# Optimization experiments

Measured on AMD Instinct MI355X. Metric: run time of the kernel, lower is better.

Reference implementation:

```python
import jax, jax.numpy as jnp
import numpy as np

B, H, W = 8, 640, 640
THRESH = 0.6       # self.threshold in Pnet_post
NMS_IOU = 0.3      # iou threshold passed in post_data_Pnet
MAX_DET = 128      # fixed detection budget (padded greedy NMS)


def _tffix(x):
    # tf fix(): floor toward zero
    return jnp.where(x >= 0, jnp.floor(x), jnp.ceil(x))


def _rec2square(rect):
    # rect: [N,5] (x1,y1,x2,y2,score) -> squared boxes
    x1, y1, x2, y2, s = rect[:, 0], rect[:, 1], rect[:, 2], rect[:, 3], rect[:, 4]
    w = x2 - x1
    h = y2 - y1
    l = jnp.maximum(w, h)
    nx1 = x1 + w * 0.5 - l * 0.5
    ny1 = y1 + h * 0.5 - l * 0.5
    return jnp.stack([nx1, ny1, nx1 + l, ny1 + l, s], axis=1)


def _greedy_nms(rect, valid):
    # rect: [N,5]; valid: [N] bool (score >= THRESH). Sequential greedy NMS
    # (highest score first, suppress iou > NMS_IOU), padded to MAX_DET rows.
    x1, y1, x2, y2 = rect[:, 0], rect[:, 1], rect[:, 2], rect[:, 3]
    area = (x2 - x1 + 1.0) * (y2 - y1 + 1.0)
    s0 = jnp.where(valid, rect[:, 4], -jnp.inf)

    def step(s, _):
        i = jnp.argmax(s)
        alive = jnp.isfinite(s[i])
        xx1 = jnp.maximum(x1[i], x1)
        yy1 = jnp.maximum(y1[i], y1)
        xx2 = jnp.minimum(x2[i], x2)
        yy2 = jnp.minimum(y2[i], y2)
        inter = jnp.maximum(0.0, xx2 - xx1 + 1.0) * jnp.maximum(0.0, yy2 - yy1 + 1.0)
        iou = inter / (area[i] + area - inter)
        s_next = jnp.where(iou > NMS_IOU, -jnp.inf, s).at[i].set(-jnp.inf)
        s_next = jnp.where(alive, s_next, s)
        return s_next, (i, alive)

    _, (picks, alive) = jax.lax.scan(step, s0, None, length=MAX_DET)
    out = rect[picks]                       # [MAX_DET,5]
    return jnp.where(alive[:, None], out, 0.0)


def _post_single(cls, roi, scale, h_raw, w_raw):
    # cls: [H,W,2], roi: [H,W,4], scale/h_raw/w_raw: scalars
    h, w = cls.shape[0], cls.shape[1]
    score = cls[:, :, 1].T                  # [W,H] == Cls_pro[...,0]
    offset = jnp.transpose(roi, (1, 0, 2))  # [W,H,4] == stacked dx1..dx4
    out_side = max(w, h)
    stride = 0.0 if out_side == 1 else (2.0 * out_side + 11.0 - 12.0) / (out_side - 1.0)
    sc = 1.0 / scale                        # scale arg of _cls_bb2rect is 1/scale
    ii = jnp.broadcast_to(jnp.arange(w, dtype=jnp.float32)[:, None], (w, h))
    jj = jnp.broadcast_to(jnp.arange(h, dtype=jnp.float32)[None, :], (w, h))
    idx = jnp.stack([ii, jj], axis=-1)      # [W,H,2] grid coords (thresh_index)
    bb1 = _tffix(stride * idx * sc)
    bb2 = _tffix((stride * idx + 11.0) * sc)
    box = jnp.concatenate([bb1, bb2], axis=-1) + offset * 12.0 * sc  # [W,H,4]
    rect = jnp.concatenate([box, score[..., None]], axis=-1).reshape(-1, 5)
    rect = _rec2square(rect)
    # pick_rect: clip to image, swap inverted corners
    x1 = jnp.maximum(0.0, rect[:, 0])
    y1 = jnp.maximum(0.0, rect[:, 1])
    x2 = jnp.minimum(w_raw, rect[:, 2])
    y2 = jnp.minimum(h_raw, rect[:, 3])
    inv = (x1 > x2) | (y1 > y2)
    fx1 = jnp.where(inv, jnp.minimum(x1, x2), x1)
    fy1 = jnp.where(inv, jnp.minimum(y1, y2), y1)
    fx2 = jnp.where(inv, jnp.maximum(x1, x2), x2)
    fy2 = jnp.where(inv, jnp.maximum(y1, y2), y2)
    pick = jnp.stack([fx1, fy1, fx2, fy2, rect[:, 4]], axis=1)
    valid = score.reshape(-1) >= THRESH     # dynamic threshold -> mask
    return _greedy_nms(pick, valid)


def setup_inputs() -> dict:
    key = jax.random.key(0)
    k1, k2, k3 = jax.random.split(key, 3)
    classifier = jax.random.uniform(k1, (B, H, W, 2), dtype=jnp.float32)
    bbox_regress = jax.random.normal(k2, (B, H, W, 4), dtype=jnp.float32) * 0.1
    scale = jax.random.uniform(k3, (B,), dtype=jnp.float32, minval=0.4, maxval=1.0)
    height_raw = jnp.full((B, 1), 1500.0, dtype=jnp.float32)
    width_raw = jnp.full((B, 1), 1500.0, dtype=jnp.float32)
    return {"classifier": classifier, "bbox_regress": bbox_regress,
            "scale": scale, "height_raw": height_raw, "width_raw": width_raw}


def reference(classifier, bbox_regress, scale, height_raw, width_raw):
    # -> [B, MAX_DET, 5]; rows beyond #detections are zero
    return jax.vmap(_post_single)(classifier, bbox_regress, scale,
                                  height_raw[:, 0], width_raw[:, 0])
```

## Files before the change

### kernel.cpp

```cpp
#include <hip/hip_runtime.h>

#define Bn 8
#define Hn 640
#define Wn 640
#define CELLS (Hn*Wn)
#define NBIN 2048
#define HB 16
#define CB 32
#define NT 5
#define TCAP 1024
#define TSTEP 832u
#define MAXD 128
#define TSTAGE 192

#define WS_CUT_BYTE 256
#define WS_PART_BYTE 512
#define WS_KEYS_BYTE (512 + Bn*HB*NBIN*2)

__global__ void k_hist(const float4* __restrict__ cls4, unsigned short* __restrict__ part) {
    __shared__ unsigned h[NBIN];
    int b = blockIdx.y, blk = blockIdx.x, tid = threadIdx.x;
    for (int p = tid; p < NBIN; p += 256) h[p] = 0u;
    __syncthreads();
    const float4* src = cls4 + ((size_t)b * CELLS + blk * (CELLS / HB)) / 2;
    for (int k = 0; k < (CELLS / HB / 2) / 256; ++k) {
        float4 v = src[k * 256 + tid];
        if (v.y >= 0.6f) {
            int bin = min((int)((v.y - 0.6f) * 5120.0f), NBIN - 1);
            atomicAdd(&h[bin], 1u);
        }
        if (v.w >= 0.6f) {
            int bin = min((int)((v.w - 0.6f) * 5120.0f), NBIN - 1);
            atomicAdd(&h[bin], 1u);
        }
    }
    __syncthreads();
    unsigned short* dst = part + (size_t)(b * HB + blk) * NBIN;
    for (int p = tid; p < NBIN; p += 256) dst[p] = (unsigned short)h[p];
}

__global__ void k_cut(const unsigned short* __restrict__ part, float* __restrict__ cutv,
                      unsigned* __restrict__ cnt) {
    __shared__ unsigned h[NBIN];
    __shared__ int best[NT];
    int b = blockIdx.x, tid = threadIdx.x;
    const int Q = NBIN / 256;
    unsigned acc[Q];
    for (int q = 0; q < Q; ++q) acc[q] = 0u;
    for (int blk = 0; blk < HB; ++blk) {
        const unsigned short* src = part + (size_t)(b * HB + blk) * NBIN;
        for (int q = 0; q < Q; ++q) acc[q] += src[q * 256 + tid];
    }
    for (int q = 0; q < Q; ++q) h[q * 256 + tid] = acc[q];
    if (tid < NT) best[tid] = 0;
    if (tid < 8) cnt[b * 8 + tid] = 0u;
    __syncthreads();
    for (int off = 1; off < NBIN; off <<= 1) {
        unsigned v[Q];
        for (int q = 0; q < Q; ++q) {
            int p = q * 256 + tid;
            v[q] = h[p] + ((p + off < NBIN) ? h[p + off] : 0u);
        }
        __syncthreads();
        for (int q = 0; q < Q; ++q) h[q * 256 + tid] = v[q];
        __syncthreads();
    }
    for (int t = 0; t < NT; ++t) {
        unsigned tgt = TSTEP * (unsigned)(t + 1);
        for (int q = 0; q < Q; ++q) {
            int p = q * 256 + tid;
            if (h[p] >= tgt && (p == NBIN - 1 || h[p + 1] < tgt)) best[t] = p;
        }
    }
    __syncthreads();
    if (tid < NT) cutv[b * 8 + tid] = 0.6f + (float)best[tid] * (0.4f / (float)NBIN);
}

__global__ void k_compact(const float4* __restrict__ cls4, const float* __restrict__ cutv_g,
                          unsigned* __restrict__ cnt, unsigned long long* __restrict__ keys) {
    __shared__ unsigned long long buf[NT][TSTAGE];
    __shared__ unsigned lcnt[NT], gbase[NT];
    int b = blockIdx.y, blk = blockIdx.x, tid = threadIdx.x;
    float c0 = cutv_g[b * 8 + 0], c1 = cutv_g[b * 8 + 1], cmid = cutv_g[b * 8 + 2],
          c3 = cutv_g[b * 8 + 3], c4 = cutv_g[b * 8 + 4];
    if (tid < NT) lcnt[tid] = 0u;
    __syncthreads();
    int cellbase = blk * (CELLS / CB);
    const float4* src = cls4 + ((size_t)b * CELLS + cellbase) / 2;
    for (int k = 0; k < (CELLS / CB / 2) / 256; ++k) {
        float4 v = src[k * 256 + tid];
        int mm = cellbase + (k * 256 + tid) * 2;
        #pragma unroll
        for (int half = 0; half < 2; ++half) {
            float s = half ? v.w : v.y;
            if (s >= c4) {
                int t = (s < c0) + (s < c1) + (s < cmid) + (s < c3);
                unsigned idx = atomicAdd(&lcnt[t], 1u);
                if (idx < TSTAGE) {
                    int m2 = mm + half;
                    int i = m2 % Wn, j = m2 / Wn;
                    unsigned n = (unsigned)(i * Hn + j);
                    buf[t][idx] = ((unsigned long long)__float_as_uint(s) << 32) |
                                  (unsigned long long)(~n);
                }
            }
        }
    }
    __syncthreads();
    if (tid < NT) gbase[tid] = atomicAdd(&cnt[b * 8 + tid], min(lcnt[tid], (unsigned)TSTAGE));
    __syncthreads();
    for (int t = 0; t < NT; ++t) {
        unsigned tot = min(lcnt[t], (unsigned)TSTAGE);
        for (unsigned i = tid; i < tot; i += 256) {
            unsigned slot = gbase[t] + i;
            if (slot < TCAP)
                keys[((size_t)b * NT + t) * TCAP + slot] = buf[t][i];
        }
    }
}

__device__ __forceinline__ void make_box(int n, float sc, float WR, float HR,
                                         const float4* __restrict__ roi4b,
                                         float& fx1, float& fy1, float& fx2, float& fy2) {
    const float stride = (float)(1279.0 / 639.0);
    int i = n / Hn, j = n % Hn;
    float fi = (float)i, fj = (float)j;
    float b1x = truncf((stride * fi) * sc);
    float b1y = truncf((stride * fj) * sc);
    float b2x = truncf((stride * fi + 11.0f) * sc);
    float b2y = truncf((stride * fj + 11.0f) * sc);
    float4 off = roi4b[j * Wn + i];
    float x1 = b1x + (off.x * 12.0f) * sc;
    float y1 = b1y + (off.y * 12.0f) * sc;
    float x2 = b2x + (off.z * 12.0f) * sc;
    float y2 = b2y + (off.w * 12.0f) * sc;
    float w = x2 - x1, h = y2 - y1;
    float l = fmaxf(w, h);
    float nx1 = x1 + w * 0.5f - l * 0.5f;
    float ny1 = y1 + h * 0.5f - l * 0.5f;
    float nx2 = nx1 + l, ny2 = ny1 + l;
    float cx1 = fmaxf(0.0f, nx1), cy1 = fmaxf(0.0f, ny1);
    float cx2 = fminf(WR, nx2),   cy2 = fminf(HR, ny2);
    bool inv = (cx1 > cx2) || (cy1 > cy2);
    fx1 = inv ? fminf(cx1, cx2) : cx1;
    fy1 = inv ? fminf(cy1, cy2) : cy1;
    fx2 = inv ? fmaxf(cx1, cx2) : cx2;
    fy2 = inv ? fmaxf(cy1, cy2) : cy2;
}

__device__ __forceinline__ void wave_phases64(unsigned long long* ks, int chunkbase,
                                              int k, int jstart) {
    int lane = threadIdx.x & 63;
    for (int j = jstart; j > 0; j >>= 1) {
        int p = chunkbase + lane;
        int ixj = p ^ j;
        if (ixj > p) {
            unsigned long long a = ks[p], c = ks[ixj];
            bool descBlk = ((p & k) == 0);
            if (descBlk ? (a < c) : (a > c)) { ks[p] = c; ks[ixj] = a; }
        }
        asm volatile("s_waitcnt lgkmcnt(0)" ::: "memory");
    }
}

__launch_bounds__(1024)
__global__ void k_nms(const float4* __restrict__ roi4, const float* __restrict__ scale,
                      const float* __restrict__ hraw, const float* __restrict__ wraw,
                      const unsigned* __restrict__ cnt,
                      const unsigned long long* __restrict__ keys_g,
                      float* __restrict__ out) {
    __shared__ unsigned long long ks[TCAP];
    __shared__ float4 bx[TCAP];
    __shared__ float4 abox[MAXD];
    __shared__ float aarea[MAXD], ascore[MAXD];
    __shared__ int sn_acc;
    int b = blockIdx.x, tid = threadIdx.x;
    int wave = tid >> 6, lane = tid & 63;
    int chunkbase = wave * 64;

    if (tid == 0) sn_acc = 0;

    float sc = 1.0f / scale[b];
    float WR = wraw[b], HR = hraw[b];
    const float4* roi4b = roi4 + (size_t)b * CELLS;

    int n_acc = 0;

    for (int t = 0; t < NT; ++t) {
        __syncthreads();
        if (sn_acc >= MAXD) break;
        int mt = (int)min(cnt[b * 8 + t], (unsigned)TCAP);
        ks[tid] = (tid < mt) ? keys_g[((size_t)b * NT + t) * TCAP + tid] : 0ULL;
        __syncthreads();

        if (mt > 1) {
            for (int k = 2; k <= 64; k <<= 1)
                wave_phases64(ks, chunkbase, k, k >> 1);
            __syncthreads();
            for (int k = 128; k <= TCAP; k <<= 1) {
                for (int j = k >> 1; j >= 64; j >>= 1) {
                    int p = tid, ixj = p ^ j;
                    if (ixj > p) {
                        unsigned long long a = ks[p], c = ks[ixj];
                        bool descBlk = ((p & k) == 0);
                        if (descBlk ? (a < c) : (a > c)) { ks[p] = c; ks[ixj] = a; }
                    }
                    __syncthreads();
                }
                wave_phases64(ks, chunkbase, k, 32);
                __syncthreads();
            }
        }

        if (tid < mt) {
            unsigned n = ~(unsigned)ks[tid];
            float fx1, fy1, fx2, fy2;
            make_box((int)n, sc, WR, HR, roi4b, fx1, fy1, fx2, fy2);
            bx[tid] = make_float4(fx1, fy1, fx2, fy2);
        }
        __syncthreads();

        if (tid < 64 && mt > 0) {
            int pos = 0;
            while (pos < mt && n_acc < MAXD) {
                int myp = pos + lane;
                bool has = myp < mt;
                unsigned long long key = has ? ks[myp] : 0ULL;
                float s = __uint_as_float((unsigned)(key >> 32));
                float4 bb0 = bx[has ? myp : 0];
                float fx1 = bb0.x, fy1 = bb0.y, fx2 = bb0.z, fy2 = bb0.w;
                float area = (fx2 - fx1 + 1.0f) * (fy2 - fy1 + 1.0f);
                bool rejected = !has;
                for (int k2 = 0; k2 < n_acc; ++k2) {
                    float4 bb = abox[k2];
                    float va = aarea[k2];
                    float iw = fminf(fx2, bb.z) - fmaxf(fx1, bb.x) + 1.0f;
                    float ih = fminf(fy2, bb.w) - fmaxf(fy1, bb.y) + 1.0f;
                    float inter = fmaxf(0.0f, iw) * fmaxf(0.0f, ih);
                    float iou = inter / (area + va - inter);
                    rejected |= (iou > 0.3f);
                }
                unsigned long long active = __ballot(!rejected);
                while (active && n_acc < MAXD) {
                    int f = __ffsll(active) - 1;
                    float bx1 = __shfl(fx1, f), by1 = __shfl(fy1, f);
                    float bx2 = __shfl(fx2, f), by2 = __shfl(fy2, f);
                    float bar = __shfl(area, f), bs = __shfl(s, f);
                    if (lane == 0) {
                        abox[n_acc] = make_float4(bx1, by1, bx2, by2);
                        aarea[n_acc] = bar;
                        ascore[n_acc] = bs;
                    }
                    if (lane == f) rejected = true;
                    if (!rejected) {
                        float iw = fminf(fx2, bx2) - fmaxf(fx1, bx1) + 1.0f;
                        float ih = fminf(fy2, by2) - fmaxf(fy1, by1) + 1.0f;
                        float inter = fmaxf(0.0f, iw) * fmaxf(0.0f, ih);
                        float iou = inter / (area + bar - inter);
                        rejected |= (iou > 0.3f);
                    }
                    n_acc++;
                    active = __ballot(!rejected);
                }
                pos += 64;
            }
            if (tid == 0) sn_acc = n_acc;
        }
    }
    __syncthreads();

    if (tid < 64) {
        for (int q = lane; q < MAXD * 5; q += 64) {
            int k2 = q / 5, c = q % 5;
            float v = 0.0f;
            if (k2 < n_acc) {
                float4 bb = abox[k2];
                v = (c == 0) ? bb.x : (c == 1) ? bb.y : (c == 2) ? bb.z
                    : (c == 3) ? bb.w : ascore[k2];
            }
            out[(b * MAXD + k2) * 5 + c] = v;
        }
    }
}

extern "C" void kernel_launch(void* const* d_in, const int* in_sizes, int n_in,
                              void* d_out, int out_size, void* d_ws, size_t ws_size,
                              hipStream_t stream) {
    const float4* cls4 = (const float4*)d_in[0];
    const float4* roi4 = (const float4*)d_in[1];
    const float* scale = (const float*)d_in[2];
    const float* hraw  = (const float*)d_in[3];
    const float* wraw  = (const float*)d_in[4];
    float* out = (float*)d_out;

    unsigned* cnt = (unsigned*)d_ws;
    float*    cutv = (float*)((char*)d_ws + WS_CUT_BYTE);
    unsigned short* part = (unsigned short*)((char*)d_ws + WS_PART_BYTE);
    unsigned long long* keys = (unsigned long long*)((char*)d_ws + WS_KEYS_BYTE);

    hipLaunchKernelGGL(k_hist, dim3(HB, Bn), dim3(256), 0, stream, cls4, part);
    hipLaunchKernelGGL(k_cut, dim3(Bn), dim3(256), 0, stream, part, cutv, cnt);
    hipLaunchKernelGGL(k_compact, dim3(CB, Bn), dim3(256), 0, stream, cls4, cutv, cnt, keys);
    hipLaunchKernelGGL(k_nms, dim3(Bn), dim3(1024), 0, stream,
                       roi4, scale, hraw, wraw, cnt, keys, out);
}
```

Measured before the change: 206.8 us.

## Parallelize NMS candidate prefilter across all waves in the block

Result: no change. 207.4 us (+0.3%).

```diff
diff --git a/kernel.cpp b/kernel.cpp
--- a/kernel.cpp
+++ b/kernel.cpp
@@ -170,7 +170,6 @@
                       const unsigned long long* __restrict__ keys_g,
                       float* __restrict__ out) {
     __shared__ unsigned long long ks[TCAP];
-    __shared__ float4 bx[TCAP];
     __shared__ float4 abox[MAXD];
     __shared__ float aarea[MAXD], ascore[MAXD];
     __shared__ int sn_acc;
@@ -184,12 +183,11 @@
     float WR = wraw[b], HR = hraw[b];
     const float4* roi4b = roi4 + (size_t)b * CELLS;
 
-    int n_acc = 0;
-
     for (int t = 0; t < NT; ++t) {
         __syncthreads();
         if (sn_acc >= MAXD) break;
         int mt = (int)min(cnt[b * 8 + t], (unsigned)TCAP);
+        if (mt == 0) continue;
         ks[tid] = (tid < mt) ? keys_g[((size_t)b * NT + t) * TCAP + tid] : 0ULL;
         __syncthreads();
 
@@ -212,26 +210,32 @@
             }
         }
 
-        if (tid < mt) {
-            unsigned n = ~(unsigned)ks[tid];
-            float fx1, fy1, fx2, fy2;
+        unsigned long long mykey = ks[tid];
+        bool has = tid < mt;
+        float fx1 = 0.f, fy1 = 0.f, fx2 = 0.f, fy2 = 0.f, area = 1.0f;
+        if (has) {
+            unsigned n = ~(unsigned)mykey;
             make_box((int)n, sc, WR, HR, roi4b, fx1, fy1, fx2, fy2);
-            bx[tid] = make_float4(fx1, fy1, fx2, fy2);
-        }
-        __syncthreads();
-
-        if (tid < 64 && mt > 0) {
-            int pos = 0;
-            while (pos < mt && n_acc < MAXD) {
-                int myp = pos + lane;
-                bool has = myp < mt;
-                unsigned long long key = has ? ks[myp] : 0ULL;
-                float s = __uint_as_float((unsigned)(key >> 32));
-                float4 bb0 = bx[has ? myp : 0];
-                float fx1 = bb0.x, fy1 = bb0.y, fx2 = bb0.z, fy2 = bb0.w;
-                float area = (fx2 - fx1 + 1.0f) * (fy2 - fy1 + 1.0f);
-                bool rejected = !has;
-                for (int k2 = 0; k2 < n_acc; ++k2) {
+            area = (fx2 - fx1 + 1.0f) * (fy2 - fy1 + 1.0f);
+        }
+        float s = __uint_as_float((unsigned)(mykey >> 32));
+
+        int n_pre = sn_acc;
+        bool rejected = !has;
+        for (int k2 = 0; k2 < n_pre; ++k2) {
+            float4 bb = abox[k2];
+            float va = aarea[k2];
+            float iw = fminf(fx2, bb.z) - fmaxf(fx1, bb.x) + 1.0f;
+            float ih = fminf(fy2, bb.w) - fmaxf(fy1, bb.y) + 1.0f;
+            float inter = fmaxf(0.0f, iw) * fmaxf(0.0f, ih);
+            float iou = inter / (area + va - inter);
+            rejected |= (iou > 0.3f);
+        }
+
+        for (int w = 0; w < 16; ++w) {
+            if (wave == w) {
+                int nacc = sn_acc;
+                for (int k2 = n_pre; k2 < nacc; ++k2) {
                     float4 bb = abox[k2];
                     float va = aarea[k2];
                     float iw = fminf(fx2, bb.z) - fmaxf(fx1, bb.x) + 1.0f;
@@ -241,15 +245,15 @@
                     rejected |= (iou > 0.3f);
                 }
                 unsigned long long active = __ballot(!rejected);
-                while (active && n_acc < MAXD) {
+                while (active && nacc < MAXD) {
                     int f = __ffsll(active) - 1;
                     float bx1 = __shfl(fx1, f), by1 = __shfl(fy1, f);
                     float bx2 = __shfl(fx2, f), by2 = __shfl(fy2, f);
                     float bar = __shfl(area, f), bs = __shfl(s, f);
                     if (lane == 0) {
-                        abox[n_acc] = make_float4(bx1, by1, bx2, by2);
-                        aarea[n_acc] = bar;
-                        ascore[n_acc] = bs;
+                        abox[nacc] = make_float4(bx1, by1, bx2, by2);
+                        aarea[nacc] = bar;
+                        ascore[nacc] = bs;
                     }
                     if (lane == f) rejected = true;
                     if (!rejected) {
@@ -259,21 +263,23 @@
                         float iou = inter / (area + bar - inter);
                         rejected |= (iou > 0.3f);
                     }
-                    n_acc++;
+                    nacc++;
                     active = __ballot(!rejected);
                 }
-                pos += 64;
+                if (lane == 0) sn_acc = nacc;
             }
-            if (tid == 0) sn_acc = n_acc;
-        }
-    }
-    __syncthreads();
-
+            __syncthreads();
+            if (sn_acc >= MAXD) break;
+        }
+    }
+    __syncthreads();
+
+    int nacc = sn_acc;
     if (tid < 64) {
         for (int q = lane; q < MAXD * 5; q += 64) {
             int k2 = q / 5, c = q % 5;
             float v = 0.0f;
-            if (k2 < n_acc) {
+            if (k2 < nacc) {
                 float4 bb = abox[k2];
                 v = (c == 0) ? bb.x : (c == 1) ? bb.y : (c == 2) ? bb.z
                     : (c == 3) ? bb.w : ascore[k2];
```
